# Performance work log

Measured on AMD Instinct MI355X. Metric: run time of the kernel, lower is better.

The kernel has to match this reference:

```python
import jax, jax.numpy as jnp
import numpy as np

NEG = -1e30  # finite stand-in for -inf (keeps logsumexp NaN-free)
B, T, V, L = 64, 1024, 512, 128
BLANK = 0


def setup_inputs() -> dict:
    key = jax.random.key(0)
    k1, k2 = jax.random.split(key)
    outputs = jax.random.normal(k1, (B, T, V), dtype=jnp.float32)
    labels = jax.random.randint(k2, (B, L), 1, V, dtype=jnp.int32)  # labels avoid blank=0
    output_lengths = jnp.full((B,), T, dtype=jnp.int32)
    label_lengths = jnp.full((B,), L, dtype=jnp.int32)
    return {"outputs": outputs, "labels": labels,
            "output_lengths": output_lengths, "label_lengths": label_lengths}


def _ctc_loss(log_probs, labels, output_lengths, label_lengths):
    # log_probs: [B, T, V]; labels: [B, L]
    S = 2 * L + 1
    # extended label sequence: blank, l1, blank, l2, ..., blank
    ext = jnp.full((B, S), BLANK, dtype=labels.dtype).at[:, 1::2].set(labels)
    # skip transition allowed at s if ext[s] != blank and ext[s] != ext[s-2]
    ext_m2 = jnp.pad(ext, ((0, 0), (2, 0)), constant_values=BLANK)[:, :S]
    skip = (ext != BLANK) & (ext != ext_m2) & (jnp.arange(S) >= 2)

    # emission log-probs on the lattice: emit[b, t, s] = log_probs[b, t, ext[b, s]]
    bidx = jnp.arange(B)
    emit = log_probs[bidx[:, None, None], jnp.arange(T)[None, :, None], ext[:, None, :]]  # [B,T,S]
    emit_t = jnp.moveaxis(emit, 1, 0)  # [T, B, S]

    alpha0 = (jnp.full((B, S), NEG, dtype=log_probs.dtype)
              .at[:, 0].set(emit_t[0, :, 0])
              .at[:, 1].set(emit_t[0, :, 1]))

    neg1 = jnp.full((B, 1), NEG, dtype=log_probs.dtype)
    neg2 = jnp.full((B, 2), NEG, dtype=log_probs.dtype)

    def step(alpha, e):
        p0 = alpha
        p1 = jnp.concatenate([neg1, alpha[:, :-1]], axis=1)
        p2 = jnp.where(skip, jnp.concatenate([neg2, alpha[:, :-2]], axis=1), NEG)
        m = jnp.maximum(p0, jnp.maximum(p1, p2))
        lse = m + jnp.log(jnp.exp(p0 - m) + jnp.exp(p1 - m) + jnp.exp(p2 - m))
        new = lse + e
        return new, new

    _, alphas = jax.lax.scan(step, alpha0, emit_t[1:])
    alphas = jnp.concatenate([alpha0[None], alphas], axis=0)  # [T, B, S]

    a_last = alphas[output_lengths - 1, bidx]  # [B, S] alpha at final frame per sample
    s1 = 2 * label_lengths      # final blank state
    s0 = 2 * label_lengths - 1  # final label state
    a0 = a_last[bidx, s0]
    a1 = a_last[bidx, s1]
    m = jnp.maximum(a0, a1)
    log_lik = m + jnp.log(jnp.exp(a0 - m) + jnp.exp(a1 - m))
    # reduction='mean': per-sample nll divided by target length, then batch mean
    loss = -log_lik / label_lengths.astype(log_lik.dtype)
    return jnp.mean(loss)


def reference(outputs, labels, output_lengths, label_lengths):
    return _ctc_loss(outputs, labels, output_lengths, label_lengths)
```

## Files before the change

### kernel.cpp

```cpp
#include <hip/hip_runtime.h>

#define B_ 64
#define T_ 1024
#define V_ 512
#define L_ 128
#define LOG2E_ 1.4426950408889634f
#define LN2_   0.6931471805599453f
#define C_ 56
#define RW4_ 65
#define NC_ ((T_ - 1 + C_ - 1) / C_)

typedef float f4_t __attribute__((ext_vector_type(4)));

__device__ __forceinline__ float exp2_fast(float x) { return __builtin_amdgcn_exp2f(x); }
__device__ __forceinline__ float log2_fast(float x) { return __builtin_amdgcn_logf(x); }
__device__ __forceinline__ float ldx(float v, int e) { return __builtin_amdgcn_ldexpf(v, e); }

__device__ __forceinline__ float dpp_shr1_f(float x) {
    return __int_as_float(__builtin_amdgcn_update_dpp(0, __float_as_int(x), 0x138, 0xf, 0xf, true));
}
__device__ __forceinline__ int dpp_shr1_i(int x) {
    return __builtin_amdgcn_update_dpp(0, x, 0x138, 0xf, 0xf, true);
}

__global__ __launch_bounds__(512, 1) void ctc_alpha_kernel(
    const float* __restrict__ outputs, const int* __restrict__ labels,
    const int* __restrict__ out_lens, const int* __restrict__ lab_lens,
    float* __restrict__ ws, float* __restrict__ out)
{
    const int b    = blockIdx.x;
    const int tid  = threadIdx.x;
    const int wid  = tid >> 6;
    const int lane = tid & 63;

    int* cnt = (int*)ws;
    float* losses = ws + 16;

    __shared__ f4_t  ring4[2][C_ * RW4_];
    __shared__ float save2[2];
    __shared__ int   saveE[2];
    __shared__ int   amLast;

    const int olen  = out_lens[b];
    const int ll    = lab_lens[b];
    const int s0q   = 2 * ll - 1;
    const int s1q   = 2 * ll;
    const int tlast = olen - 1;
    const int l0  = s0q >> 2, j0 = s0q & 3;
    const int l1e = (s1q == 256) ? 63 : (s1q >> 2);
    const int j1  = s1q & 3;
    const float* base = outputs + (size_t)b * T_ * V_;
    const int*   lab  = labels + b * L_;

    const int cA = lab[2 * lane];
    const int cB = lab[2 * lane + 1];

    float sk1 = 0.f, sk3 = 0.f;
    float v0 = 0.f, v1 = 0.f, v2 = 0.f, v3 = 0.f, vx = 0.f;
    int   E = 0;
    const bool isl0 = (lane == 0);
    if (wid == 0) {
        __builtin_amdgcn_s_setprio(3);
        sk3 = (cB != cA) ? 1.f : 0.f;
        if (lane >= 1) sk1 = (cA != lab[2 * lane - 1]) ? 1.f : 0.f;
        if (isl0) {
            v0 = exp2_fast(base[0]      * LOG2E_);
            v1 = exp2_fast(base[lab[0]] * LOG2E_);
        }
        if (tlast == 0) {
            float w0 = (j0==0)?v0:(j0==1)?v1:(j0==2)?v2:v3;
            float w1 = (s1q==256) ? vx : ((j1==0)?v0:(j1==1)?v1:(j1==2)?v2:v3);
            if (lane == l0)  { save2[0] = w0; saveE[0] = E; }
            if (lane == l1e) { save2[1] = w1; saveE[1] = E; }
        }
    } else {
        __builtin_amdgcn_s_setprio(0);
    }

    auto produce = [&](int bb, int t0) {
        float gb[8], g1[8], g3[8];
        #pragma unroll
        for (int m = 0; m < 8; ++m) {
            int t = t0 + (wid - 1) + 7 * m;
            const float* rp = (t < T_) ? (base + (size_t)t * V_) : base;
            gb[m] = rp[0];
            g1[m] = rp[cA];
            g3[m] = rp[cB];
        }
        #pragma unroll
        for (int m = 0; m < 8; ++m) {
            int r = (wid - 1) + 7 * m;
            int t = t0 + r;
            if (t < T_) {
                f4_t e;
                e.x = exp2_fast(gb[m] * LOG2E_);
                e.y = exp2_fast(g1[m] * LOG2E_);
                e.z = exp2_fast(g3[m] * LOG2E_);
                e.w = 0.f;
                ring4[bb][r * RW4_ + lane] = e;
            }
        }
    };

    auto step = [&](f4_t e) {
        float up1 = dpp_shr1_f(v3);
        int   upE = dpp_shr1_i(E);
        upE = isl0 ? E : upE;

        int d    = upE - E;
        int mpos = (d > 0) ? d : 0;
        int sin  = (d < 0) ? d : 0;
        int sown = -mpos;
        E += mpos;
        v0 = ldx(v0, sown); v1 = ldx(v1, sown); v2 = ldx(v2, sown);
        v3 = ldx(v3, sown); vx = ldx(vx, sown);
        up1 = ldx(up1, sin);

        float n0 = (v0 + up1) * e.x;
        float n1 = fmaf(sk1, up1, v1 + v0) * e.y;
        float n2 = (v2 + v1) * e.x;
        float n3 = fmaf(sk3, v1, v3 + v2) * e.z;
        vx = (vx + v3) * e.x;
        v0 = n0; v1 = n1; v2 = n2; v3 = n3;
    };

    auto renorm = [&]() {
        float mx = fmaxf(fmaxf(v0, v1), fmaxf(v2, v3));
        mx = fmaxf(mx, vx);
        int ex = (__float_as_int(mx) >> 23) - 126;
        v0 = ldx(v0, -ex); v1 = ldx(v1, -ex); v2 = ldx(v2, -ex); v3 = ldx(v3, -ex);
        vx = ldx(vx, -ex);
        E += ex;
    };

    auto consume = [&](int bb, int t0) {
        const f4_t* rp4 = &ring4[bb][lane];
        f4_t eb2[2];
        eb2[0] = rp4[0];
        eb2[1] = rp4[RW4_];

        bool chk = (t0 + C_ > T_) || ((unsigned)(tlast - t0) < (unsigned)C_);
        if (!chk) {
            #pragma unroll 8
            for (int r = 0; r < C_; ++r) {
                f4_t e = eb2[r & 1];
                if (r + 2 < C_) eb2[r & 1] = rp4[(r + 2) * RW4_];
                step(e);
                if ((r & 3) == 3) renorm();
            }
        } else {
            #pragma unroll 4
            for (int r = 0; r < C_; ++r) {
                int t = t0 + r;
                if (t >= T_) break;
                f4_t e = eb2[r & 1];
                if (r + 2 < C_) eb2[r & 1] = rp4[(r + 2) * RW4_];
                step(e);
                if ((r & 3) == 3) renorm();
                if (t == tlast) {
                    float w0 = (j0==0)?v0:(j0==1)?v1:(j0==2)?v2:v3;
                    float w1 = (s1q==256) ? vx : ((j1==0)?v0:(j1==1)?v1:(j1==2)?v2:v3);
                    if (lane == l0)  { save2[0] = w0; saveE[0] = E; }
                    if (lane == l1e) { save2[1] = w1; saveE[1] = E; }
                }
            }
        }
    };

    if (wid > 0) produce(0, 1);
    __syncthreads();
    for (int c = 0; c < NC_; ++c) {
        if (wid > 0) {
            if (c + 1 < NC_) produce((c + 1) & 1, 1 + (c + 1) * C_);
        } else {
            consume(c & 1, 1 + c * C_);
        }
        __syncthreads();
    }

    if (tid == 0) {
        float lx = log2_fast(save2[0]) + (float)saveE[0];
        float ly = log2_fast(save2[1]) + (float)saveE[1];
        float m  = fmaxf(lx, ly);
        float lik2 = m + log2_fast(exp2_fast(lx - m) + exp2_fast(ly - m));
        float loss = -(lik2 * LN2_) / (float)ll;
        __hip_atomic_store(&losses[b], loss, __ATOMIC_RELAXED, __HIP_MEMORY_SCOPE_AGENT);
        int old = __hip_atomic_fetch_add(cnt, 1, __ATOMIC_ACQ_REL, __HIP_MEMORY_SCOPE_AGENT);
        amLast = (old == B_ - 1);
    }
    __syncthreads();
    if (amLast && wid == 0) {
        float v = __hip_atomic_load(&losses[lane], __ATOMIC_RELAXED, __HIP_MEMORY_SCOPE_AGENT);
        #pragma unroll
        for (int o = 32; o > 0; o >>= 1) v += __shfl_down(v, o);
        if (lane == 0) out[0] = v * (1.0f / B_);
    }
}

extern "C" void kernel_launch(void* const* d_in, const int* in_sizes, int n_in,
                              void* d_out, int out_size, void* d_ws, size_t ws_size,
                              hipStream_t stream) {
    const float* outputs  = (const float*)d_in[0];
    const int*   labels   = (const int*)d_in[1];
    const int*   out_lens = (const int*)d_in[2];
    const int*   lab_lens = (const int*)d_in[3];

    (void)hipMemsetAsync(d_ws, 0, 64, stream);
    ctc_alpha_kernel<<<B_, 512, 0, stream>>>(outputs, labels, out_lens, lab_lens,
                                             (float*)d_ws, (float*)d_out);
}
```

Baseline: 234.3 us.

## Split time axis across four chained blocks per sample with in-block producer flags

```diff
diff --git a/kernel.cpp b/kernel.cpp
--- a/kernel.cpp
+++ b/kernel.cpp
@@ -6,24 +6,285 @@
 #define L_ 128
 #define LOG2E_ 1.4426950408889634f
 #define LN2_   0.6931471805599453f
+
+typedef float f4_t __attribute__((ext_vector_type(4)));
+typedef float f2_t __attribute__((ext_vector_type(2)));
+
+__device__ __forceinline__ float exp2_fast(float x) { return __builtin_amdgcn_exp2f(x); }
+__device__ __forceinline__ float log2_fast(float x) { return __builtin_amdgcn_logf(x); }
+__device__ __forceinline__ float ldx(float v, int e) { return __builtin_amdgcn_ldexpf(v, e); }
+
+__device__ __forceinline__ float dpp_shr1_f(float x) {
+    return __int_as_float(__builtin_amdgcn_update_dpp(0, __float_as_int(x), 0x138, 0xf, 0xf, true));
+}
+__device__ __forceinline__ int dpp_shr1_i(int x) {
+    return __builtin_amdgcn_update_dpp(0, x, 0x138, 0xf, 0xf, true);
+}
+__device__ __forceinline__ float ag_loadf(const float* p) {
+    return __hip_atomic_load((float*)p, __ATOMIC_RELAXED, __HIP_MEMORY_SCOPE_AGENT);
+}
+__device__ __forceinline__ void ag_storef(float* p, float v) {
+    __hip_atomic_store(p, v, __ATOMIC_RELAXED, __HIP_MEMORY_SCOPE_AGENT);
+}
+
+#define JB_   4
+#define RPB_  256
+#define PPB_  128
+#define PRW_  260
+#define WS_FLAG_I_ 256
+#define WS_HOFF_F_ 1024
+#define WS_NEED_   (4096 + (size_t)B_*JB_*384*4)
+
+__global__ __launch_bounds__(512, 1) void ctc_alpha_mb(
+    const float* __restrict__ outputs, const int* __restrict__ labels,
+    const int* __restrict__ out_lens, const int* __restrict__ lab_lens,
+    float* __restrict__ ws, float* __restrict__ out)
+{
+    const int j    = blockIdx.x >> 6;
+    const int b    = blockIdx.x & 63;
+    const int tid  = threadIdx.x;
+    const int wid  = tid >> 6;
+    const int lane = tid & 63;
+
+    int*   cnt    = (int*)ws;
+    float* losses = ws + 16;
+
+    __shared__ float pairbuf[PPB_ * PRW_];
+    __shared__ int   prog[8];
+    __shared__ float save2[2];
+    __shared__ int   saveE[2];
+
+    const int olen  = out_lens[b];
+    const int ll    = lab_lens[b];
+    const int s0q   = 2 * ll - 1;
+    const int s1q   = 2 * ll;
+    const int tlast = olen - 1;
+    const int l0  = s0q >> 2, j0 = s0q & 3;
+    const int l1e = (s1q == 256) ? 63 : (s1q >> 2);
+    const int j1  = s1q & 3;
+    const float* base = outputs + (size_t)b * T_ * V_;
+    const int*   lab  = labels + b * L_;
+
+    const int cA = lab[2 * lane];
+    const int cB = lab[2 * lane + 1];
+
+    if (tid < 8) prog[tid] = 0;
+    __syncthreads();
+
+    if (wid > 0) {
+        __builtin_amdgcn_s_setprio(0);
+        const int w    = wid;
+        const int segS = (w - 1) * 38;
+        const int segE = (w < 7) ? segS + 38 : RPB_;
+        for (int g = segS; g < segE; g += 8) {
+            const int n = (segE - g >= 8) ? 8 : (segE - g);
+            float gb[8], g1[8], g3[8];
+            #pragma unroll
+            for (int m = 0; m < 8; ++m) {
+                int rr = (m < n) ? (g + m) : g;
+                const float* rp = base + (size_t)(RPB_ * j + rr) * V_;
+                gb[m] = rp[0];
+                g1[m] = rp[cA];
+                g3[m] = rp[cB];
+            }
+            #pragma unroll
+            for (int m = 0; m < 8; m += 2) {
+                if (m < n) {
+                    int pr = (g + m) >> 1;
+                    f2_t* d2 = (f2_t*)&pairbuf[pr * PRW_];
+                    f2_t e1p, e3p;
+                    e1p.x = exp2_fast(g1[m] * LOG2E_);   e1p.y = exp2_fast(g1[m+1] * LOG2E_);
+                    e3p.x = exp2_fast(g3[m] * LOG2E_);   e3p.y = exp2_fast(g3[m+1] * LOG2E_);
+                    d2[1 + lane]  = e1p;
+                    d2[65 + lane] = e3p;
+                    if (lane == 0) {
+                        f2_t ebp;
+                        ebp.x = exp2_fast(gb[m] * LOG2E_); ebp.y = exp2_fast(gb[m+1] * LOG2E_);
+                        d2[0] = ebp;
+                    }
+                }
+            }
+            if (lane == 0)
+                __hip_atomic_store(&prog[w], g + n, __ATOMIC_RELEASE, __HIP_MEMORY_SCOPE_WORKGROUP);
+        }
+        return;
+    }
+
+    __builtin_amdgcn_s_setprio(3);
+
+    float sk1 = 0.f, sk3 = 0.f;
+    sk3 = (cB != cA) ? 1.f : 0.f;
+    if (lane >= 1) sk1 = (cA != lab[2 * lane - 1]) ? 1.f : 0.f;
+
+    float v0 = 0.f, v1 = 0.f, v2 = 0.f, v3 = 0.f, vx = 0.f;
+    int   E = 0;
+    const bool isl0 = (lane == 0);
+
+    const int  lim      = tlast - RPB_ * j;
+    const bool hasHere  = (lim >= 0) && (lim < RPB_);
+    const bool doPublish= (lim >= RPB_);
+    if (lim < 0) return;
+
+    int avail = 0;
+    auto ensureAvail = [&](int need) {
+        if (need < avail) return;
+        int w = need / 38 + 1; if (w > 7) w = 7;
+        int p = __hip_atomic_load(&prog[w], __ATOMIC_ACQUIRE, __HIP_MEMORY_SCOPE_WORKGROUP);
+        while (p <= need) {
+            __builtin_amdgcn_s_sleep(2);
+            p = __hip_atomic_load(&prog[w], __ATOMIC_ACQUIRE, __HIP_MEMORY_SCOPE_WORKGROUP);
+        }
+        avail = p;
+    };
+
+    auto step = [&](float eb, float e1, float e3) {
+        float up1 = dpp_shr1_f(v3);
+        int   upE = dpp_shr1_i(E);
+        upE = isl0 ? E : upE;
+        int d    = upE - E;
+        int mpos = (d > 0) ? d : 0;
+        int sin  = (d < 0) ? d : 0;
+        int sown = -mpos;
+        E += mpos;
+        v0 = ldx(v0, sown); v1 = ldx(v1, sown); v2 = ldx(v2, sown);
+        v3 = ldx(v3, sown); vx = ldx(vx, sown);
+        up1 = ldx(up1, sin);
+        float n0 = (v0 + up1) * eb;
+        float n1 = fmaf(sk1, up1, v1 + v0) * e1;
+        float n2 = (v2 + v1) * eb;
+        float n3 = fmaf(sk3, v1, v3 + v2) * e3;
+        vx = (vx + v3) * eb;
+        v0 = n0; v1 = n1; v2 = n2; v3 = n3;
+    };
+    auto renorm = [&]() {
+        float mx = fmaxf(fmaxf(v0, v1), fmaxf(v2, v3));
+        mx = fmaxf(mx, vx);
+        int ex = (__float_as_int(mx) >> 23) - 126;
+        v0 = ldx(v0, -ex); v1 = ldx(v1, -ex); v2 = ldx(v2, -ex); v3 = ldx(v3, -ex);
+        vx = ldx(vx, -ex);
+        E += ex;
+    };
+    auto saveState = [&]() {
+        float w0 = (j0==0)?v0:(j0==1)?v1:(j0==2)?v2:v3;
+        float w1 = (s1q==256) ? vx : ((j1==0)?v0:(j1==1)?v1:(j1==2)?v2:v3);
+        if (lane == l0)  { save2[0] = w0; saveE[0] = E; }
+        if (lane == l1e) { save2[1] = w1; saveE[1] = E; }
+    };
+    auto doRowDirect = [&](int r) {
+        ensureAvail(r);
+        const float* d = &pairbuf[(r >> 1) * PRW_];
+        float eb = d[r & 1];
+        float e1 = d[2   + 2*lane + (r & 1)];
+        float e3 = d[130 + 2*lane + (r & 1)];
+        step(eb, e1, e3);
+        if ((r & 3) == 3) renorm();
+        if (r == lim) saveState();
+    };
+
+    int loopStart;
+    if (j == 0) {
+        v0 = exp2_fast(base[0]      * LOG2E_);
+        v1 = exp2_fast(base[lab[0]] * LOG2E_);
+        v0 = isl0 ? v0 : 0.f;
+        v1 = isl0 ? v1 : 0.f;
+        if (tlast == 0) saveState();
+        if (lim >= 1) doRowDirect(1);
+        if (lim >= 2) doRowDirect(2);
+        if (lim >= 3) doRowDirect(3);
+        loopStart = 2;
+    } else {
+        int* flag = (int*)ws + WS_FLAG_I_ + b * JB_ + (j - 1);
+        if (lane == 0) {
+            while (__hip_atomic_load(flag, __ATOMIC_ACQUIRE, __HIP_MEMORY_SCOPE_AGENT) == 0)
+                __builtin_amdgcn_s_sleep(4);
+        }
+        const float* h = ws + WS_HOFF_F_ + (size_t)(b * JB_ + (j - 1)) * 384 + lane * 6;
+        v0 = ag_loadf(h + 0); v1 = ag_loadf(h + 1); v2 = ag_loadf(h + 2);
+        v3 = ag_loadf(h + 3); vx = ag_loadf(h + 4);
+        E  = __float_as_int(ag_loadf(h + 5));
+        loopStart = 0;
+    }
+
+    const int fp = doPublish ? PPB_ : (lim >> 1);
+    const f2_t* pb2 = (const f2_t*)&pairbuf[0];
+
+    if (fp > loopStart) {
+        f2_t rEB0, rE10, rE30, rEB1, rE11, rE31;
+        ensureAvail(2 * loopStart + 3);
+        rEB0 = pb2[loopStart*130];       rE10 = pb2[loopStart*130 + 1 + lane];       rE30 = pb2[loopStart*130 + 65 + lane];
+        rEB1 = pb2[(loopStart+1)*130];   rE11 = pb2[(loopStart+1)*130 + 1 + lane];   rE31 = pb2[(loopStart+1)*130 + 65 + lane];
+
+        int pp = loopStart;
+        #pragma unroll 2
+        for (; pp + 1 < fp; pp += 2) {
+            {
+                f2_t eb = rEB0, e1 = rE10, e3 = rE30;
+                int pn = pp + 2;
+                if (pn < PPB_) {
+                    ensureAvail(2 * pn + 1);
+                    rEB0 = pb2[pn*130]; rE10 = pb2[pn*130 + 1 + lane]; rE30 = pb2[pn*130 + 65 + lane];
+                }
+                step(eb.x, e1.x, e3.x);
+                step(eb.y, e1.y, e3.y);
+            }
+            {
+                f2_t eb = rEB1, e1 = rE11, e3 = rE31;
+                int pn = pp + 3;
+                if (pn < PPB_) {
+                    ensureAvail(2 * pn + 1);
+                    rEB1 = pb2[pn*130]; rE11 = pb2[pn*130 + 1 + lane]; rE31 = pb2[pn*130 + 65 + lane];
+                }
+                step(eb.x, e1.x, e3.x);
+                step(eb.y, e1.y, e3.y);
+                renorm();
+            }
+        }
+        if (pp < fp) {
+            f2_t eb = rEB0, e1 = rE10, e3 = rE30;
+            step(eb.x, e1.x, e3.x);
+            step(eb.y, e1.y, e3.y);
+        }
+    }
+
+    if (hasHere) {
+        int rs = 2 * fp;
+        if (j == 0 && rs < 4) rs = 4;
+        for (int r = rs; r <= lim; ++r) doRowDirect(r);
+
+        int am = 0;
+        if (lane == 0) {
+            float lx = log2_fast(save2[0]) + (float)saveE[0];
+            float ly = log2_fast(save2[1]) + (float)saveE[1];
+            float m  = fmaxf(lx, ly);
+            float lik2 = m + log2_fast(exp2_fast(lx - m) + exp2_fast(ly - m));
+            float loss = -(lik2 * LN2_) / (float)ll;
+            ag_storef(&losses[b], loss);
+            int old = __hip_atomic_fetch_add(cnt, 1, __ATOMIC_ACQ_REL, __HIP_MEMORY_SCOPE_AGENT);
+            am = (old == B_ - 1);
+        }
+        am = __shfl(am, 0);
+        if (am) {
+            float v = ag_loadf(&losses[lane]);
+            #pragma unroll
+            for (int o = 32; o > 0; o >>= 1) v += __shfl_down(v, o);
+            if (lane == 0) out[0] = v * (1.0f / B_);
+        }
+    } else if (doPublish) {
+        float* h = ws + WS_HOFF_F_ + (size_t)(b * JB_ + j) * 384 + lane * 6;
+        ag_storef(h + 0, v0); ag_storef(h + 1, v1); ag_storef(h + 2, v2);
+        ag_storef(h + 3, v3); ag_storef(h + 4, vx);
+        ag_storef(h + 5, __int_as_float(E));
+        if (lane == 0)
+            __hip_atomic_store((int*)ws + WS_FLAG_I_ + b * JB_ + j, 1,
+                               __ATOMIC_RELEASE, __HIP_MEMORY_SCOPE_AGENT);
+    }
+}
+
 #define C_ 56
 #define RW4_ 65
 #define NC_ ((T_ - 1 + C_ - 1) / C_)
 
-typedef float f4_t __attribute__((ext_vector_type(4)));
-
-__device__ __forceinline__ float exp2_fast(float x) { return __builtin_amdgcn_exp2f(x); }
-__device__ __forceinline__ float log2_fast(float x) { return __builtin_amdgcn_logf(x); }
-__device__ __forceinline__ float ldx(float v, int e) { return __builtin_amdgcn_ldexpf(v, e); }
-
-__device__ __forceinline__ float dpp_shr1_f(float x) {
-    return __int_as_float(__builtin_amdgcn_update_dpp(0, __float_as_int(x), 0x138, 0xf, 0xf, true));
-}
-__device__ __forceinline__ int dpp_shr1_i(int x) {
-    return __builtin_amdgcn_update_dpp(0, x, 0x138, 0xf, 0xf, true);
-}
-
-__global__ __launch_bounds__(512, 1) void ctc_alpha_kernel(
+__global__ __launch_bounds__(512, 1) void ctc_alpha_fb(
     const float* __restrict__ outputs, const int* __restrict__ labels,
     const int* __restrict__ out_lens, const int* __restrict__ lab_lens,
     float* __restrict__ ws, float* __restrict__ out)
@@ -83,9 +344,7 @@
         for (int m = 0; m < 8; ++m) {
             int t = t0 + (wid - 1) + 7 * m;
             const float* rp = (t < T_) ? (base + (size_t)t * V_) : base;
-            gb[m] = rp[0];
-            g1[m] = rp[cA];
-            g3[m] = rp[cB];
+            gb[m] = rp[0]; g1[m] = rp[cA]; g3[m] = rp[cB];
         }
         #pragma unroll
         for (int m = 0; m < 8; ++m) {
@@ -106,7 +365,6 @@
         float up1 = dpp_shr1_f(v3);
         int   upE = dpp_shr1_i(E);
         upE = isl0 ? E : upE;
-
         int d    = upE - E;
         int mpos = (d > 0) ? d : 0;
         int sin  = (d < 0) ? d : 0;
@@ -115,7 +373,6 @@
         v0 = ldx(v0, sown); v1 = ldx(v1, sown); v2 = ldx(v2, sown);
         v3 = ldx(v3, sown); vx = ldx(vx, sown);
         up1 = ldx(up1, sin);
-
         float n0 = (v0 + up1) * e.x;
         float n1 = fmaf(sk1, up1, v1 + v0) * e.y;
         float n2 = (v2 + v1) * e.x;
@@ -138,7 +395,6 @@
         f4_t eb2[2];
         eb2[0] = rp4[0];
         eb2[1] = rp4[RW4_];
-
         bool chk = (t0 + C_ > T_) || ((unsigned)(tlast - t0) < (unsigned)C_);
         if (!chk) {
             #pragma unroll 8
@@ -205,7 +461,13 @@
     const int*   out_lens = (const int*)d_in[2];
     const int*   lab_lens = (const int*)d_in[3];
 
-    (void)hipMemsetAsync(d_ws, 0, 64, stream);
-    ctc_alpha_kernel<<<B_, 512, 0, stream>>>(outputs, labels, out_lens, lab_lens,
+    if (ws_size >= WS_NEED_) {
+        (void)hipMemsetAsync(d_ws, 0, 2048, stream);
+        ctc_alpha_mb<<<B_ * JB_, 512, 0, stream>>>(outputs, labels, out_lens, lab_lens,
+                                                   (float*)d_ws, (float*)d_out);
+    } else {
+        (void)hipMemsetAsync(d_ws, 0, 64, stream);
+        ctc_alpha_fb<<<B_, 512, 0, stream>>>(outputs, labels, out_lens, lab_lens,
                                              (float*)d_ws, (float*)d_out);
-}
+    }
+}
```

New measurement: 630.8 us. 2.69x slower.
